# Performance work log

Measured on AMD Instinct MI355X. Metric: run time of the kernel, lower is better.

Reference implementation:

```python
import jax, jax.numpy as jnp
import numpy as np

B, L, D = 2, 2048, 1024
NH, KVH, DH = 16, 8, 64
GROUPS = NH // KVH
ROPE_THETA = 10000.0
SPARSITY = 0.5


def setup_inputs() -> dict:
    key = jax.random.key(0)
    ks = jax.random.split(key, 5)
    hidden_states = jax.random.normal(ks[0], (B, L, D), dtype=jnp.float32)
    wq = jax.random.normal(ks[1], (D, NH * DH), dtype=jnp.float32) * 0.02
    wk = jax.random.normal(ks[2], (D, KVH * DH), dtype=jnp.float32) * 0.02
    wv = jax.random.normal(ks[3], (D, KVH * DH), dtype=jnp.float32) * 0.02
    wo = jax.random.normal(ks[4], (NH * DH, D), dtype=jnp.float32) * 0.02
    position_ids = jnp.broadcast_to(jnp.arange(L, dtype=jnp.int64 if jax.config.jax_enable_x64 else jnp.int32), (B, L))
    return {"hidden_states": hidden_states, "wq": wq, "wk": wk, "wv": wv, "wo": wo,
            "position_ids": position_ids}


def _rope_cos_sin(position_ids, dh, theta):
    inv_freq = 1.0 / (theta ** (jnp.arange(0, dh, 2, dtype=jnp.float32) / dh))  # [dh/2]
    freqs = position_ids.astype(jnp.float32)[..., None] * inv_freq              # [B,L,dh/2]
    emb = jnp.concatenate([freqs, freqs], axis=-1)                              # [B,L,dh]
    return jnp.cos(emb)[:, None], jnp.sin(emb)[:, None]                         # [B,1,L,dh]


def _rotate_half(x):
    h = x.shape[-1] // 2
    return jnp.concatenate([-x[..., h:], x[..., :h]], axis=-1)


def _attention(hidden_states, wq, wk, wv, wo, position_ids):
    b, l, _ = hidden_states.shape
    q = (hidden_states @ wq).reshape(b, l, NH, DH).transpose(0, 2, 1, 3)    # [B,NH,L,DH]
    k = (hidden_states @ wk).reshape(b, l, KVH, DH).transpose(0, 2, 1, 3)   # [B,KVH,L,DH]
    v = (hidden_states @ wv).reshape(b, l, KVH, DH).transpose(0, 2, 1, 3)

    cos, sin = _rope_cos_sin(position_ids, DH, ROPE_THETA)
    q = q * cos + _rotate_half(q) * sin
    k = k * cos + _rotate_half(k) * sin

    # repeat_kv: expand kv heads to match query heads (interleaved like torch)
    k = jnp.repeat(k, GROUPS, axis=1)
    v = jnp.repeat(v, GROUPS, axis=1)

    scale = DH ** -0.5
    scores = jnp.einsum("bhqd,bhkd->bhqk", q, k) * scale                    # [B,NH,L,L]

    # dynamic sparsity: keep exactly top_k entries per row (scatter mask, like torch)
    top_k = max(1, int(SPARSITY * l))
    flat = scores.reshape(-1, l)                                            # [N,L]
    _, idx = jax.lax.top_k(flat, top_k)                                     # [N,k]
    rows = jnp.arange(flat.shape[0])[:, None]
    mask = jnp.zeros(flat.shape, dtype=bool).at[rows, idx].set(True)
    min_val = jnp.finfo(flat.dtype).min
    sparse = jnp.where(mask, flat, min_val).reshape(scores.shape)

    probs = jax.nn.softmax(sparse.astype(jnp.float32), axis=-1).astype(q.dtype)
    out = jnp.einsum("bhqk,bhkd->bhqd", probs, v)                            # [B,NH,L,DH]
    out = out.transpose(0, 2, 1, 3).reshape(b, l, NH * DH)
    return out @ wo


def reference(hidden_states, wq, wk, wv, wo, position_ids):
    return _attention(hidden_states, wq, wk, wv, wo, position_ids)
```

## Files before the change

### kernel.cpp

```cpp
#include <hip/hip_runtime.h>
#include <cstdint>
#include <cstddef>

typedef unsigned int u32;
typedef unsigned long long u64;
typedef __attribute__((ext_vector_type(8))) short s8v;
typedef __attribute__((ext_vector_type(4))) float f4v;
typedef __attribute__((ext_vector_type(4))) unsigned short us4;

#define B_   2
#define L_   2048
#define D_   1024
#define NH_  16
#define KVH_ 8
#define DH_  64
#define TOPK_ 1024

#define MFMA16(a, b, c) __builtin_amdgcn_mfma_f32_16x16x32_bf16(a, b, c, 0, 0, 0)

__device__ __forceinline__ u32 fkey(float s) {
    u32 b = __float_as_uint(s);
    return b ^ ((u32)((int)b >> 31) | 0x80000000u);
}
__device__ __forceinline__ float fkeyinv(u32 k) {
    u32 b = (k & 0x80000000u) ? (k ^ 0x80000000u) : ~k;
    return __uint_as_float(b);
}
__device__ __forceinline__ unsigned short bf16rne(float x) {
    u32 u = __float_as_uint(x);
    u32 r = (u + 0x7FFFu + ((u >> 16) & 1u)) >> 16;
    return (unsigned short)r;
}
__device__ __forceinline__ float bf2f(unsigned short h) {
    return __uint_as_float((u32)h << 16);
}

__global__ __launch_bounds__(256) void prep_wt(const float* __restrict__ W,
                                               unsigned short* __restrict__ WtH,
                                               unsigned short* __restrict__ WtL,
                                               int K, int N) {
    __shared__ float tile[64 * 65];
    int k0 = blockIdx.x * 64, n0 = blockIdx.y * 64;
    int t = threadIdx.x;
#pragma unroll
    for (int i = 0; i < 16; ++i) {
        int idx = t + i * 256;
        int kk = idx >> 6, nn = idx & 63;
        tile[kk * 65 + nn] = W[(size_t)(k0 + kk) * N + n0 + nn];
    }
    __syncthreads();
#pragma unroll
    for (int i = 0; i < 16; ++i) {
        int idx = t + i * 256;
        int nn = idx >> 6, kk = idx & 63;
        float x = tile[kk * 65 + nn];
        unsigned short hi = bf16rne(x);
        unsigned short lo = bf16rne(x - bf2f(hi));
        WtH[(size_t)(n0 + nn) * K + k0 + kk] = hi;
        WtL[(size_t)(n0 + nn) * K + k0 + kk] = lo;
    }
}

__global__ __launch_bounds__(256) void split_a(const float* __restrict__ A,
                                               unsigned short* __restrict__ AH,
                                               unsigned short* __restrict__ AL) {
    size_t tid = (size_t)blockIdx.x * 256 + threadIdx.x;
    float4 v = *(const float4*)(A + tid * 4);
    us4 hv, lv;
    float x[4] = {v.x, v.y, v.z, v.w};
#pragma unroll
    for (int i = 0; i < 4; ++i) {
        unsigned short hi = bf16rne(x[i]);
        hv[i] = hi;
        lv[i] = bf16rne(x[i] - bf2f(hi));
    }
    *(us4*)(AH + tid * 4) = hv;
    *(us4*)(AL + tid * 4) = lv;
}

__global__ __launch_bounds__(256) void gemm_bf(
    const unsigned short* __restrict__ Ah,
    const unsigned short* __restrict__ Al,
    int lda,
    const unsigned short* __restrict__ Wh,
    const unsigned short* __restrict__ Wl,
    float* __restrict__ C, int K, int N) {
    __shared__ __align__(16) unsigned short lAh[128 * 40];
    __shared__ __align__(16) unsigned short lAl[128 * 40];
    __shared__ __align__(16) unsigned short lBh[128 * 40];
    __shared__ __align__(16) unsigned short lBl[128 * 40];
    const int t = threadIdx.x, lane = t & 63, w = t >> 6;
    const int quad = lane >> 4, col = lane & 15;
    const int wm = w >> 1, wn = w & 1;
    const int nwg = gridDim.x * gridDim.y;
    const int lin = blockIdx.y * gridDim.x + blockIdx.x;
    const int swz = (lin & 7) * (nwg >> 3) + (lin >> 3);
    const int bx = swz % gridDim.x, by = swz / gridDim.x;
    const int m0 = bx * 128, n0 = by * 128;
    const int sr = t >> 1, sk = (t & 1) * 16;

    f4v acc[4][4];
#pragma unroll
    for (int i = 0; i < 4; ++i)
#pragma unroll
        for (int j = 0; j < 4; ++j) acc[i][j] = (f4v){0.f, 0.f, 0.f, 0.f};

    for (int k0 = 0; k0 < K; k0 += 32) {
        const unsigned short* ap = Ah + (size_t)(m0 + sr) * lda + k0 + sk;
        const unsigned short* alp = Al + (size_t)(m0 + sr) * lda + k0 + sk;
        s8v a_h0 = *(const s8v*)(ap);
        s8v a_h1 = *(const s8v*)(ap + 8);
        s8v a_l0 = *(const s8v*)(alp);
        s8v a_l1 = *(const s8v*)(alp + 8);
        s8v bh0 = *(const s8v*)(Wh + (size_t)(n0 + sr) * K + k0 + sk);
        s8v bh1 = *(const s8v*)(Wh + (size_t)(n0 + sr) * K + k0 + sk + 8);
        s8v bl0 = *(const s8v*)(Wl + (size_t)(n0 + sr) * K + k0 + sk);
        s8v bl1 = *(const s8v*)(Wl + (size_t)(n0 + sr) * K + k0 + sk + 8);
        __syncthreads();
        *(s8v*)&lAh[sr * 40 + sk]     = a_h0;
        *(s8v*)&lAh[sr * 40 + sk + 8] = a_h1;
        *(s8v*)&lAl[sr * 40 + sk]     = a_l0;
        *(s8v*)&lAl[sr * 40 + sk + 8] = a_l1;
        *(s8v*)&lBh[sr * 40 + sk]     = bh0;
        *(s8v*)&lBh[sr * 40 + sk + 8] = bh1;
        *(s8v*)&lBl[sr * 40 + sk]     = bl0;
        *(s8v*)&lBl[sr * 40 + sk + 8] = bl1;
        __syncthreads();
        s8v amh[4], aml[4], bnh[4], bnl[4];
#pragma unroll
        for (int mt = 0; mt < 4; ++mt) {
            amh[mt] = *(s8v*)&lAh[(wm * 64 + mt * 16 + col) * 40 + quad * 8];
            aml[mt] = *(s8v*)&lAl[(wm * 64 + mt * 16 + col) * 40 + quad * 8];
        }
#pragma unroll
        for (int nt = 0; nt < 4; ++nt) {
            bnh[nt] = *(s8v*)&lBh[(wn * 64 + nt * 16 + col) * 40 + quad * 8];
            bnl[nt] = *(s8v*)&lBl[(wn * 64 + nt * 16 + col) * 40 + quad * 8];
        }
#pragma unroll
        for (int mt = 0; mt < 4; ++mt)
#pragma unroll
            for (int nt = 0; nt < 4; ++nt) {
                acc[mt][nt] = MFMA16(amh[mt], bnh[nt], acc[mt][nt]);
                acc[mt][nt] = MFMA16(amh[mt], bnl[nt], acc[mt][nt]);
                acc[mt][nt] = MFMA16(aml[mt], bnh[nt], acc[mt][nt]);
            }
    }
#pragma unroll
    for (int mt = 0; mt < 4; ++mt)
#pragma unroll
        for (int nt = 0; nt < 4; ++nt)
#pragma unroll
            for (int r = 0; r < 4; ++r)
                C[(size_t)(m0 + wm * 64 + mt * 16 + quad * 4 + r) * N +
                  n0 + wn * 64 + nt * 16 + col] = acc[mt][nt][r];
}

__global__ __launch_bounds__(256) void rope_q(float* __restrict__ Q,
                                              const int* __restrict__ pos) {
    int tid = blockIdx.x * 256 + threadIdx.x;
    int dl = tid & 31;
    int h  = (tid >> 5) & 15;
    int l  = (tid >> 9) & 2047;
    int b  = tid >> 20;
    size_t base = (size_t)(b * L_ + l) * 2048 + h * DH_;
    float x1 = Q[base + dl];
    float x2 = Q[base + dl + 32];
    float p = (float)pos[b * L_ + l];
    float invf = (float)pow(10000.0, -(double)dl / 32.0);
    float a = p * invf;
    float s, c;
    sincosf(a, &s, &c);
    Q[base + dl]      = x1 * c - x2 * s;
    Q[base + dl + 32] = x2 * c + x1 * s;
}

__global__ __launch_bounds__(256) void prep_k(const float* __restrict__ QKV,
                                              unsigned short* __restrict__ KHp,
                                              unsigned short* __restrict__ KLp,
                                              const int* __restrict__ pos) {
    int tid = blockIdx.x * 256 + threadIdx.x;
    int d   = tid & 63;
    int l   = (tid >> 6) & 2047;
    int kvh = (tid >> 17) & 7;
    int b   = tid >> 20;
    size_t src = (size_t)(b * L_ + l) * 2048 + 1024 + kvh * DH_;
    float x  = QKV[src + d];
    int dp   = (d < 32) ? d + 32 : d - 32;
    float xp = QKV[src + dp];
    float p = (float)pos[b * L_ + l];
    int i = d & 31;
    float invf = (float)pow(10000.0, -(double)i / 32.0);
    float a = p * invf;
    float s, c;
    sincosf(a, &s, &c);
    float out = (d < 32) ? (x * c - xp * s) : (x * c + xp * s);
    unsigned short hi = bf16rne(out);
    unsigned short lo = bf16rne(out - bf2f(hi));
    size_t dst = ((size_t)(b * KVH_ + kvh) * L_ + l) * DH_ + d;
    KHp[dst] = hi;
    KLp[dst] = lo;
}

__global__ __launch_bounds__(256) void prep_v(const float* __restrict__ QKV,
                                              unsigned short* __restrict__ VTp) {
    __shared__ float tile[64 * 65];
    int bid = blockIdx.x;
    int lb  = bid & 31;
    int kvh = (bid >> 5) & 7;
    int b   = bid >> 8;
    int l0  = lb * 64;
    int t   = threadIdx.x;
#pragma unroll
    for (int i = 0; i < 16; ++i) {
        int idx = t + i * 256;
        int ll = idx >> 6, d = idx & 63;
        tile[ll * 65 + d] =
            QKV[(size_t)(b * L_ + l0 + ll) * 2048 + 1536 + kvh * DH_ + d];
    }
    __syncthreads();
#pragma unroll
    for (int i = 0; i < 16; ++i) {
        int idx = t + i * 256;
        int d = idx >> 6, ll = idx & 63;
        VTp[((size_t)(b * KVH_ + kvh) * DH_ + d) * L_ + l0 + ll] = bf16rne(tile[ll * 65 + d]);
    }
}

__global__ __launch_bounds__(512, 4) void attn(
    const float* __restrict__ QR,
    const unsigned short* __restrict__ KH,
    const unsigned short* __restrict__ KL,
    const unsigned short* __restrict__ VT,
    unsigned short* __restrict__ AOus) {

    extern __shared__ __align__(16) unsigned char dynsm[];
    float* Sc = (float*)dynsm;
    unsigned short* Pc = (unsigned short*)dynsm;
    u32* hist = (u32*)(dynsm + 66304);
    float* qtile  = (float*)(dynsm + 74496);
    float* outred = (float*)(dynsm + 74496);

    const int t = threadIdx.x;
    const int lane = t & 63, w = t >> 6;
    const int quad = lane >> 4, col = lane & 15;
    const int bid0 = blockIdx.x;
    const int bid  = (bid0 & 7) * 512 + (bid0 >> 3);
    const int l0  = (bid & 255) * 8;
    const int kvh = (bid >> 8) & 7;
    const int b   = bid >> 11;
    const int r0 = 2 * w, r1 = 2 * w + 1;

    if (t < 256) {
        int q = t >> 4, d4 = (t & 15) * 4;
        *(float4*)&qtile[q * 68 + d4] =
            *(const float4*)(QR + (size_t)(b * L_ + l0 + (q & 7)) * 2048 +
                             (kvh * 2 + (q >> 3)) * DH_ + d4);
    }
    __syncthreads();

    union FR { s8v v; unsigned short u[8]; };
    FR ah[2], al[2];
#pragma unroll
    for (int ks = 0; ks < 2; ++ks)
#pragma unroll
        for (int i = 0; i < 8; ++i) {
            float x = qtile[col * 68 + ks * 32 + quad * 8 + i];
            unsigned short hi = bf16rne(x);
            ah[ks].u[i] = hi;
            al[ks].u[i] = bf16rne(x - bf2f(hi));
        }

    const size_t slabK = (size_t)(b * KVH_ + kvh) * L_ * DH_;
    const unsigned short* khp = KH + slabK;
    const unsigned short* klp = KL + slabK;
    u32 ukA[32], ukB[32];

#pragma unroll
    for (int half = 0; half < 2; ++half) {
        if (half) __syncthreads();
#pragma unroll
        for (int tj = 0; tj < 8; ++tj) {
            int jl = w * 128 + tj * 16;
            int j0 = half * 1024 + jl;
            const unsigned short* kh8 = khp + (size_t)(j0 + col) * 64 + quad * 8;
            const unsigned short* kl8 = klp + (size_t)(j0 + col) * 64 + quad * 8;
            s8v bh0 = *(const s8v*)(kh8);
            s8v bh1 = *(const s8v*)(kh8 + 32);
            s8v bl0 = *(const s8v*)(kl8);
            s8v bl1 = *(const s8v*)(kl8 + 32);
            f4v c = {0.f, 0.f, 0.f, 0.f};
            c = MFMA16(ah[0].v, bh0, c);
            c = MFMA16(al[0].v, bh0, c);
            c = MFMA16(ah[0].v, bl0, c);
            c = MFMA16(ah[1].v, bh1, c);
            c = MFMA16(al[1].v, bh1, c);
            c = MFMA16(ah[1].v, bl1, c);
            c = c * 0.125f;
#pragma unroll
            for (int r = 0; r < 4; ++r)
                Sc[(quad * 4 + r) * 1034 + jl + col] = c[r];
        }
        __syncthreads();
        if (half == 0) {
            outred[t] = 0.f;
            outred[t + 512] = 0.f;
            if (t < 64) outred[1024 + t] = 0.f;
        }
#pragma unroll
        for (int i2 = 0; i2 < 16; ++i2) {
            ukA[half * 16 + i2] = fkey(Sc[r0 * 1034 + i2 * 64 + lane]);
            ukB[half * 16 + i2] = fkey(Sc[r1 * 1034 + i2 * 64 + lane]);
        }
    }
    __syncthreads();

    u32* hq = &hist[w * 256];
    auto middle = [&](u32 (&uk)[32]) -> float {
        u32 ulo = 0xFFFFFFFFu, uhi = 0u;
#pragma unroll
        for (int i = 0; i < 32; ++i) {
            u32 u = uk[i];
            ulo = (u < ulo) ? u : ulo;
            uhi = (u > uhi) ? u : uhi;
        }
        for (int off = 1; off < 64; off <<= 1) {
            u32 ol = (u32)__shfl_xor((int)ulo, off);
            u32 oh = (u32)__shfl_xor((int)uhi, off);
            ulo = (ol < ulo) ? ol : ulo;
            uhi = (oh > uhi) ? oh : uhi;
        }
        const float mrow = fkeyinv(uhi);
        const int sh = __clz((int)((uhi - ulo) | 1u));
#pragma unroll
        for (int i = 0; i < 32; ++i) uk[i] = (uk[i] - ulo) << sh;

        u32 pf = 0u, kq = (u32)TOPK_, ng = 0u, geq = 0u;
        for (int pass = 0; pass < 4; ++pass) {
            int shift = 24 - 8 * pass;
#pragma unroll
            for (int i = 0; i < 4; ++i) hq[i * 64 + lane] = 0u;
            u32 pm = pass ? (0xFFFFFFFFu << (shift + 8)) : 0u;
#pragma unroll
            for (int i = 0; i < 32; ++i) {
                u32 u = uk[i];
                if ((u & pm) == pf) {
                    u32 d = (u >> shift) & 255u;
                    atomicAdd(&hq[(d & 3) * 64 + (d >> 2)], 1u);
                }
            }
            u32 h0 = hq[0 * 64 + lane], h1 = hq[1 * 64 + lane];
            u32 h2 = hq[2 * 64 + lane], h3 = hq[3 * 64 + lane];
            u32 s4 = h0 + h1 + h2 + h3;
            u32 v = s4;
            for (int off = 1; off < 64; off <<= 1) {
                u32 tmp = __shfl_down(v, off);
                if (lane + off < 64) v += tmp;
            }
            u32 g = v - s4;
            u32 hb_[4] = {h0, h1, h2, h3};
            u32 mydig = 0u, myk = 0u, myng = 0u, myhb = 0u;
            bool found = false;
#pragma unroll
            for (int bb = 3; bb >= 0; --bb) {
                u32 hb = hb_[bb];
                if (hb && g < kq && kq <= g + hb) {
                    found = true;
                    mydig = (u32)(4 * lane + bb);
                    myk   = kq - g;
                    myng  = ng + g;
                    myhb  = hb;
                }
                g += hb;
            }
            u64 fm = __ballot(found);
            int src = (int)__builtin_ctzll(fm);
            pf |= ((u32)__shfl((int)mydig, src)) << shift;
            kq  = (u32)__shfl((int)myk,  src);
            ng  = (u32)__shfl((int)myng, src);
            u32 hbs = (u32)__shfl((int)myhb, src);
            if (kq == hbs) { geq = 1u; break; }
        }

        const u32 uth = pf;
        u32 selm = 0u;
        if (geq) {
#pragma unroll
            for (int i = 0; i < 32; ++i)
                if (uk[i] >= uth) selm |= 1u << i;
        } else {
            const u32 quota = (u32)TOPK_ - ng;
            u32 eqm = 0u;
#pragma unroll
            for (int i = 0; i < 32; ++i) {
                u32 u = uk[i];
                if (u > uth) selm |= 1u << i;
                else if (u == uth) eqm |= 1u << i;
            }
            u32 ec = (u32)__builtin_popcount(eqm);
            for (int off = 1; off < 64; off <<= 1) ec += __shfl_xor(ec, off);
            if (ec == quota) {
                selm |= eqm;
            } else {
                u32 base = 0;
                u64 lmask = ((u64)1 << lane) - 1;
#pragma unroll
                for (int i = 0; i < 32; ++i) {
                    u64 mm = __ballot((eqm >> i) & 1u);
                    if ((eqm >> i) & 1u) {
                        u32 rk = base + (u32)__builtin_popcountll(mm & lmask);
                        if (rk < quota) selm |= 1u << i;
                    }
                    base += (u32)__builtin_popcountll(mm);
                }
            }
        }

        float z = 0.f;
#pragma unroll
        for (int i = 0; i < 32; ++i) {
            float vv = fkeyinv((uk[i] >> sh) + ulo);
            float e = ((selm >> i) & 1u) ? __expf(vv - mrow) : 0.f;
            uk[i] = __float_as_uint(e);
            z += e;
        }
        for (int off = 1; off < 64; off <<= 1) z += __shfl_xor(z, off);
        return 1.0f / z;
    };

    float invZA = middle(ukA);
    float invZB = middle(ukB);

    const unsigned short* vt = VT + (size_t)(b * KVH_ + kvh) * DH_ * L_;
    const int jb0 = w * 256 + quad * 8;
    s8v pv0 = *(const s8v*)(vt + (size_t)( 0 + col) * L_ + jb0);
    s8v pv1 = *(const s8v*)(vt + (size_t)(16 + col) * L_ + jb0);
    s8v pv2 = *(const s8v*)(vt + (size_t)(32 + col) * L_ + jb0);
    s8v pv3 = *(const s8v*)(vt + (size_t)(48 + col) * L_ + jb0);

#pragma unroll
    for (int i = 0; i < 32; ++i) {
        int jp = 1024 * (i >> 4) + 64 * (i & 15) + lane;
        Pc[r0 * 2072 + jp] = bf16rne(__uint_as_float(ukA[i]) * invZA);
        Pc[r1 * 2072 + jp] = bf16rne(__uint_as_float(ukB[i]) * invZB);
    }
    __syncthreads();

    f4v acc0 = {0.f, 0.f, 0.f, 0.f}, acc1 = acc0, acc2 = acc0, acc3 = acc0;
    {
        s8v ap = *(const s8v*)&Pc[col * 2072 + jb0];
        acc0 = MFMA16(ap, pv0, acc0);
        acc1 = MFMA16(ap, pv1, acc1);
        acc2 = MFMA16(ap, pv2, acc2);
        acc3 = MFMA16(ap, pv3, acc3);
    }
#pragma unroll
    for (int kc = 1; kc < 8; ++kc) {
        int jb = w * 256 + kc * 32 + quad * 8;
        s8v ap = *(const s8v*)&Pc[col * 2072 + jb];
        s8v v0 = *(const s8v*)(vt + (size_t)( 0 + col) * L_ + jb);
        s8v v1 = *(const s8v*)(vt + (size_t)(16 + col) * L_ + jb);
        s8v v2 = *(const s8v*)(vt + (size_t)(32 + col) * L_ + jb);
        s8v v3 = *(const s8v*)(vt + (size_t)(48 + col) * L_ + jb);
        acc0 = MFMA16(ap, v0, acc0);
        acc1 = MFMA16(ap, v1, acc1);
        acc2 = MFMA16(ap, v2, acc2);
        acc3 = MFMA16(ap, v3, acc3);
    }

#pragma unroll
    for (int r = 0; r < 4; ++r) {
        atomicAdd(&outred[(quad * 4 + r) * 68 +  0 + col], acc0[r]);
        atomicAdd(&outred[(quad * 4 + r) * 68 + 16 + col], acc1[r]);
        atomicAdd(&outred[(quad * 4 + r) * 68 + 32 + col], acc2[r]);
        atomicAdd(&outred[(quad * 4 + r) * 68 + 48 + col], acc3[r]);
    }
    __syncthreads();
    if (t < 256) {
        int q = t >> 4, d4 = (t & 15) * 4;
        float4 o = *(float4*)&outred[q * 68 + d4];
        size_t m = (size_t)(b * L_ + l0 + (q & 7));
        int n = (kvh * 2 + (q >> 3)) * DH_ + d4;
        float x[4] = {o.x, o.y, o.z, o.w};
        us4 hv, lv;
#pragma unroll
        for (int i = 0; i < 4; ++i) {
            unsigned short hi = bf16rne(x[i]);
            hv[i] = hi;
            lv[i] = bf16rne(x[i] - bf2f(hi));
        }
        *(us4*)(AOus + m * 4096 + 2048 + n) = hv;
        *(us4*)(AOus + m * 4096 + 3072 + n) = lv;
    }
}

extern "C" void kernel_launch(void* const* d_in, const int* in_sizes, int n_in,
                              void* d_out, int out_size, void* d_ws, size_t ws_size,
                              hipStream_t stream) {
    const float* hs = (const float*)d_in[0];
    const float* wq = (const float*)d_in[1];
    const float* wk = (const float*)d_in[2];
    const float* wv = (const float*)d_in[3];
    const float* wo = (const float*)d_in[4];
    const int*  pos = (const int*)d_in[5];

    float* ws = (float*)d_ws;
    const size_t M1 = 1u << 20;
    float* QKV = ws;
    unsigned short* QKVWh = (unsigned short*)(ws +  8 * M1);
    unsigned short* QKVWl = (unsigned short*)(ws +  9 * M1);
    unsigned short* WoH   = (unsigned short*)(ws + 10 * M1);
    unsigned short* WoL   = (unsigned short*)(ws + 10 * M1 + M1 / 2);
    unsigned short* KH    = (unsigned short*)(ws + 11 * M1);
    unsigned short* KL    = (unsigned short*)(ws + 12 * M1);
    unsigned short* VT    = (unsigned short*)(ws + 13 * M1);
    unsigned short* hsH   = (unsigned short*)(ws + 11 * M1);
    unsigned short* hsL   = (unsigned short*)(ws + 13 * M1);
    float* out = (float*)d_out;

    static bool attr_set = false;
    if (!attr_set) {
        hipFuncSetAttribute((const void*)attn,
                            hipFuncAttributeMaxDynamicSharedMemorySize, 78848);
        attr_set = true;
    }

    dim3 blk(256);
    prep_wt<<<dim3(16, 16), blk, 0, stream>>>(wq, QKVWh, QKVWl, 1024, 1024);
    prep_wt<<<dim3(16,  8), blk, 0, stream>>>(wk, QKVWh + (size_t)1024 * 1024,
                                              QKVWl + (size_t)1024 * 1024, 1024, 512);
    prep_wt<<<dim3(16,  8), blk, 0, stream>>>(wv, QKVWh + (size_t)1536 * 1024,
                                              QKVWl + (size_t)1536 * 1024, 1024, 512);
    prep_wt<<<dim3(16, 16), blk, 0, stream>>>(wo, WoH, WoL, 1024, 1024);
    split_a<<<dim3(4096), blk, 0, stream>>>(hs, hsH, hsL);
    gemm_bf<<<dim3(32, 16), blk, 0, stream>>>(hsH, hsL, 1024, QKVWh, QKVWl,
                                              QKV, 1024, 2048);
    rope_q<<<dim3(8192), blk, 0, stream>>>(QKV, pos);
    prep_k<<<dim3(8192), blk, 0, stream>>>(QKV, KH, KL, pos);
    prep_v<<<dim3(512),  blk, 0, stream>>>(QKV, VT);
    attn<<<dim3(4096), dim3(512), 78848, stream>>>(QKV, KH, KL, VT,
                                                   (unsigned short*)QKV);
    gemm_bf<<<dim3(32, 8), blk, 0, stream>>>((unsigned short*)QKV + 2048,
                                             (unsigned short*)QKV + 3072, 4096,
                                             WoH, WoL, out, 1024, 1024);
}
```

Before: 824.1 us.

## Split attention blocks per query head instead of per KV-head group

Each attention block now handles 8 query rows of a single query head rather than 16 rows covering both heads that share a KV head. Each wave owns one row instead of two, which halves the score registers and shared memory per block (and raises the launch-bounds occupancy hint from 4 to 6). The grid doubles to 8192 blocks. In exchange, the MFMA tiles are half wasted because the 16-row A operand duplicates the 8 query rows, and K/V loads are repeated per head, doubling K/V traffic and MFMA work per query.

```diff
diff --git a/kernel.cpp b/kernel.cpp
--- a/kernel.cpp
+++ b/kernel.cpp
@@ -227,7 +227,7 @@
     }
 }
 
-__global__ __launch_bounds__(512, 4) void attn(
+__global__ __launch_bounds__(512, 6) void attn(
     const float* __restrict__ QR,
     const unsigned short* __restrict__ KH,
     const unsigned short* __restrict__ KL,
@@ -237,25 +237,24 @@
     extern __shared__ __align__(16) unsigned char dynsm[];
     float* Sc = (float*)dynsm;
     unsigned short* Pc = (unsigned short*)dynsm;
-    u32* hist = (u32*)(dynsm + 66304);
-    float* qtile  = (float*)(dynsm + 74496);
-    float* outred = (float*)(dynsm + 74496);
+    u32* hist = (u32*)(dynsm + 33152);
+    float* qtile  = (float*)(dynsm + 41344);
+    float* outred = (float*)(dynsm + 41344);
 
     const int t = threadIdx.x;
     const int lane = t & 63, w = t >> 6;
     const int quad = lane >> 4, col = lane & 15;
     const int bid0 = blockIdx.x;
-    const int bid  = (bid0 & 7) * 512 + (bid0 >> 3);
-    const int l0  = (bid & 255) * 8;
-    const int kvh = (bid >> 8) & 7;
-    const int b   = bid >> 11;
-    const int r0 = 2 * w, r1 = 2 * w + 1;
-
-    if (t < 256) {
+    const int bid  = (bid0 & 7) * 1024 + (bid0 >> 3);
+    const int l0 = (bid & 255) * 8;
+    const int h  = (bid >> 8) & 15;
+    const int b  = bid >> 12;
+    const int kvh = h >> 1;
+
+    if (t < 128) {
         int q = t >> 4, d4 = (t & 15) * 4;
         *(float4*)&qtile[q * 68 + d4] =
-            *(const float4*)(QR + (size_t)(b * L_ + l0 + (q & 7)) * 2048 +
-                             (kvh * 2 + (q >> 3)) * DH_ + d4);
+            *(const float4*)(QR + (size_t)(b * L_ + l0 + q) * 2048 + h * DH_ + d4);
     }
     __syncthreads();
 
@@ -265,7 +264,7 @@
     for (int ks = 0; ks < 2; ++ks)
 #pragma unroll
         for (int i = 0; i < 8; ++i) {
-            float x = qtile[col * 68 + ks * 32 + quad * 8 + i];
+            float x = qtile[(col & 7) * 68 + ks * 32 + quad * 8 + i];
             unsigned short hi = bf16rne(x);
             ah[ks].u[i] = hi;
             al[ks].u[i] = bf16rne(x - bf2f(hi));
@@ -274,7 +273,7 @@
     const size_t slabK = (size_t)(b * KVH_ + kvh) * L_ * DH_;
     const unsigned short* khp = KH + slabK;
     const unsigned short* klp = KL + slabK;
-    u32 ukA[32], ukB[32];
+    u32 uk[32];
 
 #pragma unroll
     for (int half = 0; half < 2; ++half) {
@@ -297,26 +296,26 @@
             c = MFMA16(al[1].v, bh1, c);
             c = MFMA16(ah[1].v, bl1, c);
             c = c * 0.125f;
-#pragma unroll
-            for (int r = 0; r < 4; ++r)
-                Sc[(quad * 4 + r) * 1034 + jl + col] = c[r];
+            if (quad < 2) {
+#pragma unroll
+                for (int r = 0; r < 4; ++r)
+                    Sc[(quad * 4 + r) * 1034 + jl + col] = c[r];
+            }
         }
         __syncthreads();
         if (half == 0) {
             outred[t] = 0.f;
-            outred[t + 512] = 0.f;
-            if (t < 64) outred[1024 + t] = 0.f;
-        }
-#pragma unroll
-        for (int i2 = 0; i2 < 16; ++i2) {
-            ukA[half * 16 + i2] = fkey(Sc[r0 * 1034 + i2 * 64 + lane]);
-            ukB[half * 16 + i2] = fkey(Sc[r1 * 1034 + i2 * 64 + lane]);
-        }
+            if (t < 32) outred[512 + t] = 0.f;
+        }
+#pragma unroll
+        for (int i2 = 0; i2 < 16; ++i2)
+            uk[half * 16 + i2] = fkey(Sc[w * 1034 + i2 * 64 + lane]);
     }
     __syncthreads();
 
     u32* hq = &hist[w * 256];
-    auto middle = [&](u32 (&uk)[32]) -> float {
+    float invZ;
+    {
         u32 ulo = 0xFFFFFFFFu, uhi = 0u;
 #pragma unroll
         for (int i = 0; i < 32; ++i) {
@@ -425,11 +424,8 @@
             z += e;
         }
         for (int off = 1; off < 64; off <<= 1) z += __shfl_xor(z, off);
-        return 1.0f / z;
-    };
-
-    float invZA = middle(ukA);
-    float invZB = middle(ukB);
+        invZ = 1.0f / z;
+    }
 
     const unsigned short* vt = VT + (size_t)(b * KVH_ + kvh) * DH_ * L_;
     const int jb0 = w * 256 + quad * 8;
@@ -441,14 +437,13 @@
 #pragma unroll
     for (int i = 0; i < 32; ++i) {
         int jp = 1024 * (i >> 4) + 64 * (i & 15) + lane;
-        Pc[r0 * 2072 + jp] = bf16rne(__uint_as_float(ukA[i]) * invZA);
-        Pc[r1 * 2072 + jp] = bf16rne(__uint_as_float(ukB[i]) * invZB);
+        Pc[w * 2072 + jp] = bf16rne(__uint_as_float(uk[i]) * invZ);
     }
     __syncthreads();
 
     f4v acc0 = {0.f, 0.f, 0.f, 0.f}, acc1 = acc0, acc2 = acc0, acc3 = acc0;
     {
-        s8v ap = *(const s8v*)&Pc[col * 2072 + jb0];
+        s8v ap = *(const s8v*)&Pc[(col & 7) * 2072 + jb0];
         acc0 = MFMA16(ap, pv0, acc0);
         acc1 = MFMA16(ap, pv1, acc1);
         acc2 = MFMA16(ap, pv2, acc2);
@@ -457,7 +452,7 @@
 #pragma unroll
     for (int kc = 1; kc < 8; ++kc) {
         int jb = w * 256 + kc * 32 + quad * 8;
-        s8v ap = *(const s8v*)&Pc[col * 2072 + jb];
+        s8v ap = *(const s8v*)&Pc[(col & 7) * 2072 + jb];
         s8v v0 = *(const s8v*)(vt + (size_t)( 0 + col) * L_ + jb);
         s8v v1 = *(const s8v*)(vt + (size_t)(16 + col) * L_ + jb);
         s8v v2 = *(const s8v*)(vt + (size_t)(32 + col) * L_ + jb);
@@ -468,19 +463,21 @@
         acc3 = MFMA16(ap, v3, acc3);
     }
 
-#pragma unroll
-    for (int r = 0; r < 4; ++r) {
-        atomicAdd(&outred[(quad * 4 + r) * 68 +  0 + col], acc0[r]);
-        atomicAdd(&outred[(quad * 4 + r) * 68 + 16 + col], acc1[r]);
-        atomicAdd(&outred[(quad * 4 + r) * 68 + 32 + col], acc2[r]);
-        atomicAdd(&outred[(quad * 4 + r) * 68 + 48 + col], acc3[r]);
+    if (quad < 2) {
+#pragma unroll
+        for (int r = 0; r < 4; ++r) {
+            atomicAdd(&outred[(quad * 4 + r) * 68 +  0 + col], acc0[r]);
+            atomicAdd(&outred[(quad * 4 + r) * 68 + 16 + col], acc1[r]);
+            atomicAdd(&outred[(quad * 4 + r) * 68 + 32 + col], acc2[r]);
+            atomicAdd(&outred[(quad * 4 + r) * 68 + 48 + col], acc3[r]);
+        }
     }
     __syncthreads();
-    if (t < 256) {
+    if (t < 128) {
         int q = t >> 4, d4 = (t & 15) * 4;
         float4 o = *(float4*)&outred[q * 68 + d4];
-        size_t m = (size_t)(b * L_ + l0 + (q & 7));
-        int n = (kvh * 2 + (q >> 3)) * DH_ + d4;
+        size_t m = (size_t)(b * L_ + l0 + q);
+        int n = h * DH_ + d4;
         float x[4] = {o.x, o.y, o.z, o.w};
         us4 hv, lv;
 #pragma unroll
@@ -521,7 +518,7 @@
     static bool attr_set = false;
     if (!attr_set) {
         hipFuncSetAttribute((const void*)attn,
-                            hipFuncAttributeMaxDynamicSharedMemorySize, 78848);
+                            hipFuncAttributeMaxDynamicSharedMemorySize, 43520);
         attr_set = true;
     }
 
@@ -538,7 +535,7 @@
     rope_q<<<dim3(8192), blk, 0, stream>>>(QKV, pos);
     prep_k<<<dim3(8192), blk, 0, stream>>>(QKV, KH, KL, pos);
     prep_v<<<dim3(512),  blk, 0, stream>>>(QKV, VT);
-    attn<<<dim3(4096), dim3(512), 78848, stream>>>(QKV, KH, KL, VT,
+    attn<<<dim3(8192), dim3(512), 43520, stream>>>(QKV, KH, KL, VT,
                                                    (unsigned short*)QKV);
     gemm_bf<<<dim3(32, 8), blk, 0, stream>>>((unsigned short*)QKV + 2048,
                                              (unsigned short*)QKV + 3072, 4096,
```

Measured after the change: 1.167 ms. +41.7%, slower.
